# Kernel optimization log

Hardware: AMD Instinct MI355X
Metric: run time of the kernel (lower is better)

## Reference

```python
import jax, jax.numpy as jnp
import numpy as np
import math

SEQ_LEN = 2048
EMB = 1024
HEAD = 64
BATCH = 8

def setup_inputs() -> dict:
    key = jax.random.key(0)
    k1, k2, k3, k4 = jax.random.split(key, 4)
    x = jax.random.normal(k1, (BATCH, SEQ_LEN, EMB), dtype=jnp.float32)
    # torch Linear(no bias): out = x @ W.T with W [out,in]; store as [in,out]
    s = 1.0 / math.sqrt(EMB)
    Wk = jax.random.uniform(k2, (EMB, HEAD), dtype=jnp.float32, minval=-s, maxval=s)
    Wq = jax.random.uniform(k3, (EMB, HEAD), dtype=jnp.float32, minval=-s, maxval=s)
    Wv = jax.random.uniform(k4, (EMB, HEAD), dtype=jnp.float32, minval=-s, maxval=s)
    return {"x": x, "Wk": Wk, "Wq": Wq, "Wv": Wv}

def reference(x, Wk, Wq, Wv):
    B, S, E = x.shape
    H = Wk.shape[1]
    k = x @ Wk  # [B,S,H]
    q = x @ Wq
    v = x @ Wv
    scores = jnp.einsum('bsh,bth->bst', q, k) / math.sqrt(H)
    causal = jnp.tril(jnp.ones((S, S), dtype=bool))
    scores = jnp.where(causal[None], scores, -jnp.inf)
    attn = jax.nn.softmax(scores, axis=-1)
    # dropout is identity in eval mode
    return jnp.einsum('bst,bth->bsh', attn, v)
```

## Files before the change

### kernel.cpp

```cpp
#include <hip/hip_runtime.h>
#include <hip/hip_bf16.h>

typedef __attribute__((ext_vector_type(8))) short short8;
typedef __attribute__((ext_vector_type(4))) short short4v;
typedef __attribute__((ext_vector_type(4))) float floatx4;

#define SEQ   2048
#define EMB   1024
#define HEAD  64
#define BATCH 8

__device__ __forceinline__ short f2bf(float f) {
    union { float f; unsigned u; } a; a.f = f;
    unsigned u = a.u;
    u = (u + 0x7FFFu + ((u >> 16) & 1u)) >> 16;
    return (short)u;
}

__device__ __forceinline__ void gld16(const void* g, void* l) {
    __builtin_amdgcn_global_load_lds(
        (const __attribute__((address_space(1))) unsigned int*)g,
        (__attribute__((address_space(3))) unsigned int*)l,
        16, 0, 0);
}

__global__ void wtrans_kernel(const float* __restrict__ Wk,
                              const float* __restrict__ Wq,
                              const float* __restrict__ Wv,
                              short* __restrict__ Wf) {
    int gid  = blockIdx.x * 256 + threadIdx.x;
    int lane = gid & 63;
    int fid  = gid >> 6;
    int chunk = fid & 31;
    int mnt  = fid >> 5;
    int mat  = mnt >> 2, nt = mnt & 3;
    const float* src = (mat == 0) ? Wq : (mat == 1) ? Wk : Wv;
    int n = lane & 15, quad = lane >> 4;
    int h = nt * 16 + n;
    short8 o8;
    #pragma unroll
    for (int j = 0; j < 8; ++j)
        o8[j] = f2bf(src[(chunk * 32 + quad * 8 + j) * 64 + h]);
    *(short8*)(Wf + (long)gid * 8) = o8;
}

__global__ __launch_bounds__(256, 1) void qkv_kernel(const float* __restrict__ x,
                                                     const short* __restrict__ Wf,
                                                     short* __restrict__ q,
                                                     short* __restrict__ k,
                                                     short* __restrict__ vt) {
    __shared__ short LW[2][12][4][64][8];
    const int wv   = threadIdx.x >> 6;
    const int lane = threadIdx.x & 63;
    const int l15  = lane & 15;
    const int quad = lane >> 4;
    const int row0 = blockIdx.x * 64 + wv * 16;

    floatx4 acc[12];
    #pragma unroll
    for (int f = 0; f < 12; ++f) acc[f] = (floatx4){0.f, 0.f, 0.f, 0.f};

    const float* xrow = x + (long)(row0 + l15) * EMB + quad * 8;

    #pragma unroll
    for (int i = 0; i < 12; ++i) {
        const int s = wv * 12 + i, mnt = s >> 2, c = s & 3;
        gld16(Wf + (long)(mnt * 32 + c) * 512 + lane * 8, &LW[0][mnt][c][0][0]);
    }
    __syncthreads();

    #pragma unroll 1
    for (int g = 0; g < 8; ++g) {
        const int bb = g & 1;
        const float* xg = xrow + g * 128;
        floatx4 xv[8];
        #pragma unroll
        for (int c = 0; c < 4; ++c) {
            xv[2 * c]     = *(const floatx4*)(xg + c * 32);
            xv[2 * c + 1] = *(const floatx4*)(xg + c * 32 + 4);
        }
        if (g < 7) {
            #pragma unroll
            for (int i = 0; i < 12; ++i) {
                const int s = wv * 12 + i, mnt = s >> 2, c = s & 3;
                gld16(Wf + (long)(mnt * 32 + (g + 1) * 4 + c) * 512 + lane * 8,
                      &LW[bb ^ 1][mnt][c][0][0]);
            }
        }
        #pragma unroll
        for (int c = 0; c < 4; ++c) {
            short8 a;
            #pragma unroll
            for (int i = 0; i < 4; ++i) {
                a[i]     = f2bf(xv[2 * c][i]);
                a[4 + i] = f2bf(xv[2 * c + 1][i]);
            }
            #pragma unroll
            for (int f = 0; f < 12; ++f) {
                short8 bf = *(const short8*)&LW[bb][f][c][lane][0];
                acc[f] = __builtin_amdgcn_mfma_f32_16x16x32_bf16(a, bf, acc[f], 0, 0, 0);
            }
        }
        __syncthreads();
    }

    const int bidx = row0 >> 11;
    const int srow = (row0 & (SEQ - 1)) + quad * 4;
    #pragma unroll
    for (int nt = 0; nt < 4; ++nt) {
        const int col = nt * 16 + l15;
        #pragma unroll
        for (int r = 0; r < 4; ++r) {
            long grow = (long)(row0 + quad * 4 + r);
            q[grow * HEAD + col] = f2bf(acc[nt][r]);
            k[grow * HEAD + col] = f2bf(acc[4 + nt][r]);
        }
        short4v vv;
        #pragma unroll
        for (int r = 0; r < 4; ++r) vv[r] = f2bf(acc[8 + nt][r]);
        *(short4v*)(vt + ((long)bidx * HEAD + col) * SEQ + srow) = vv;
    }
}

__global__ __launch_bounds__(256, 2) void attn_kernel(const short* __restrict__ q,
                                                      const short* __restrict__ k,
                                                      const short* __restrict__ vt,
                                                      float* __restrict__ out) {
    __shared__ short KV[2][16][64][8];
    __shared__ short Plds[4][16][40];
    __shared__ float oT[2][2][16][64];
    __shared__ float lT[2][2][16];

    const int wv   = threadIdx.x >> 6;
    const int lane = threadIdx.x & 63;
    const int l15  = lane & 15;
    const int quad = lane >> 4;
    const int rg   = wv & 1;
    const int kh   = wv >> 1;
    const int b    = blockIdx.x & 7;
    const int p    = blockIdx.x >> 3;
    const int t2   = 63 - p;
    const int s1   = p * 32, s2 = t2 * 32;
    const int nch1 = (p >> 1) + 1;
    const int nch2 = (t2 >> 1) + 1;

    const short* kbase = k  + (long)b * SEQ * HEAD;
    const short* vbase = vt + (long)b * HEAD * SEQ;

    const short* q1p = q + ((long)b * SEQ + s1 + rg * 16 + l15) * HEAD + quad * 8;
    const short* q2p = q + ((long)b * SEQ + s2 + rg * 16 + l15) * HEAD + quad * 8;
    short8 q1f0 = *(const short8*)(q1p), q1f1 = *(const short8*)(q1p + 32);
    short8 q2f0 = *(const short8*)(q2p), q2f1 = *(const short8*)(q2p + 32);

    floatx4 o1[4], o2[4];
    #pragma unroll
    for (int nh = 0; nh < 4; ++nh) {
        o1[nh] = (floatx4){0.f, 0.f, 0.f, 0.f};
        o2[nh] = (floatx4){0.f, 0.f, 0.f, 0.f};
    }
    float l1[4] = {0.f, 0.f, 0.f, 0.f};
    float l2[4] = {0.f, 0.f, 0.f, 0.f};

    auto stage = [&](int ch, int bb) {
        const int j0 = ch * 64;
        #pragma unroll
        for (int i = 0; i < 2; ++i) {
            const int fid = wv + i * 4;
            const int ntg = fid >> 1, ks = fid & 1;
            gld16(kbase + (long)(j0 + ntg * 16 + l15) * HEAD + ks * 32 + quad * 8,
                  &KV[bb][fid][0][0]);
        }
        #pragma unroll
        for (int i = 0; i < 2; ++i) {
            const int fid = wv + i * 4;
            const int kh2 = fid >> 2, nth = fid & 3;
            gld16(vbase + (long)(nth * 16 + l15) * SEQ + j0 + kh2 * 32 + quad * 8,
                  &KV[bb][8 + fid][0][0]);
        }
    };

    stage(0, 0);
    __syncthreads();

    #pragma unroll 1
    for (int ch = 0; ch < nch2; ++ch) {
        const int bb = ch & 1;
        if (ch + 1 < nch2) stage(ch + 1, bb ^ 1);
        const int j0 = ch * 64;

        short8 kf[2][2], vf[4];
        #pragma unroll
        for (int nt = 0; nt < 2; ++nt)
            #pragma unroll
            for (int ks = 0; ks < 2; ++ks)
                kf[nt][ks] = *(const short8*)&KV[bb][(kh * 2 + nt) * 2 + ks][lane][0];
        #pragma unroll
        for (int nh = 0; nh < 4; ++nh)
            vf[nh] = *(const short8*)&KV[bb][8 + kh * 4 + nh][lane][0];

        {
            floatx4 sa[2];
            sa[0] = (floatx4){0.f, 0.f, 0.f, 0.f};
            sa[1] = (floatx4){0.f, 0.f, 0.f, 0.f};
            #pragma unroll
            for (int nt = 0; nt < 2; ++nt) {
                sa[nt] = __builtin_amdgcn_mfma_f32_16x16x32_bf16(q2f0, kf[nt][0], sa[nt], 0, 0, 0);
                sa[nt] = __builtin_amdgcn_mfma_f32_16x16x32_bf16(q2f1, kf[nt][1], sa[nt], 0, 0, 0);
            }
            #pragma unroll
            for (int r = 0; r < 4; ++r) {
                const int sq = s2 + rg * 16 + quad * 4 + r;
                #pragma unroll
                for (int nt = 0; nt < 2; ++nt) {
                    const int sk = j0 + kh * 32 + nt * 16 + l15;
                    float pv = (sk > sq) ? 0.f : __expf(sa[nt][r] * 0.125f - 16.f);
                    sa[nt][r] = pv;
                    l2[r] += pv;
                }
            }
            #pragma unroll
            for (int nt = 0; nt < 2; ++nt)
                #pragma unroll
                for (int r = 0; r < 4; ++r)
                    Plds[wv][quad * 4 + r][nt * 16 + l15] = f2bf(sa[nt][r]);
            short8 pf = *(const short8*)(&Plds[wv][l15][quad * 8]);
            #pragma unroll
            for (int nh = 0; nh < 4; ++nh)
                o2[nh] = __builtin_amdgcn_mfma_f32_16x16x32_bf16(pf, vf[nh], o2[nh], 0, 0, 0);
        }

        if (ch < nch1) {
            floatx4 sa[2];
            sa[0] = (floatx4){0.f, 0.f, 0.f, 0.f};
            sa[1] = (floatx4){0.f, 0.f, 0.f, 0.f};
            #pragma unroll
            for (int nt = 0; nt < 2; ++nt) {
                sa[nt] = __builtin_amdgcn_mfma_f32_16x16x32_bf16(q1f0, kf[nt][0], sa[nt], 0, 0, 0);
                sa[nt] = __builtin_amdgcn_mfma_f32_16x16x32_bf16(q1f1, kf[nt][1], sa[nt], 0, 0, 0);
            }
            #pragma unroll
            for (int r = 0; r < 4; ++r) {
                const int sq = s1 + rg * 16 + quad * 4 + r;
                #pragma unroll
                for (int nt = 0; nt < 2; ++nt) {
                    const int sk = j0 + kh * 32 + nt * 16 + l15;
                    float pv = (sk > sq) ? 0.f : __expf(sa[nt][r] * 0.125f - 16.f);
                    sa[nt][r] = pv;
                    l1[r] += pv;
                }
            }
            #pragma unroll
            for (int nt = 0; nt < 2; ++nt)
                #pragma unroll
                for (int r = 0; r < 4; ++r)
                    Plds[wv][quad * 4 + r][nt * 16 + l15] = f2bf(sa[nt][r]);
            short8 pf = *(const short8*)(&Plds[wv][l15][quad * 8]);
            #pragma unroll
            for (int nh = 0; nh < 4; ++nh)
                o1[nh] = __builtin_amdgcn_mfma_f32_16x16x32_bf16(pf, vf[nh], o1[nh], 0, 0, 0);
        }
        __syncthreads();
    }

    #pragma unroll
    for (int msk = 1; msk <= 8; msk <<= 1) {
        #pragma unroll
        for (int r = 0; r < 4; ++r) {
            l1[r] += __shfl_xor(l1[r], msk, 64);
            l2[r] += __shfl_xor(l2[r], msk, 64);
        }
    }

    if (kh == 1) {
        #pragma unroll
        for (int nh = 0; nh < 4; ++nh)
            #pragma unroll
            for (int r = 0; r < 4; ++r) {
                oT[0][rg][quad * 4 + r][nh * 16 + l15] = o1[nh][r];
                oT[1][rg][quad * 4 + r][nh * 16 + l15] = o2[nh][r];
            }
        if (l15 == 0) {
            #pragma unroll
            for (int r = 0; r < 4; ++r) {
                lT[0][rg][quad * 4 + r] = l1[r];
                lT[1][rg][quad * 4 + r] = l2[r];
            }
        }
    }
    __syncthreads();
    if (kh == 0) {
        #pragma unroll
        for (int r = 0; r < 4; ++r) {
            const int row = quad * 4 + r;
            const float inv1 = 1.f / (l1[r] + lT[0][rg][row]);
            const float inv2 = 1.f / (l2[r] + lT[1][rg][row]);
            #pragma unroll
            for (int nh = 0; nh < 4; ++nh) {
                const int col = nh * 16 + l15;
                out[((long)b * SEQ + s1 + rg * 16 + row) * HEAD + col] =
                    (o1[nh][r] + oT[0][rg][row][col]) * inv1;
                out[((long)b * SEQ + s2 + rg * 16 + row) * HEAD + col] =
                    (o2[nh][r] + oT[1][rg][row][col]) * inv2;
            }
        }
    }
}

extern "C" void kernel_launch(void* const* d_in, const int* in_sizes, int n_in,
                              void* d_out, int out_size, void* d_ws, size_t ws_size,
                              hipStream_t stream) {
    const float* x  = (const float*)d_in[0];
    const float* Wk = (const float*)d_in[1];
    const float* Wq = (const float*)d_in[2];
    const float* Wv = (const float*)d_in[3];
    float* out = (float*)d_out;

    short* Wf = (short*)d_ws;
    short* q  = Wf + 3 * HEAD * EMB;
    short* k  = q + (long)BATCH * SEQ * HEAD;
    short* vt = k + (long)BATCH * SEQ * HEAD;

    hipLaunchKernelGGL(wtrans_kernel, dim3(96), dim3(256), 0, stream, Wk, Wq, Wv, Wf);
    hipLaunchKernelGGL(qkv_kernel, dim3(BATCH * SEQ / 64), dim3(256), 0, stream, x, Wf, q, k, vt);
    hipLaunchKernelGGL(attn_kernel, dim3(BATCH * 32), dim3(256), 0, stream, q, k, vt, out);
}
```

Measured before the change: 158.4 us.

## Split QKV projection across waves per 16-row block and unpair attention tiles

The QKV projection kernel now gives each block 16 rows, with each wave computing 3 of the 12 output tiles. B fragments are read directly from global memory, replacing the LDS double-buffered staging, and the weight layout is reordered to suit. The attention kernel no longer pairs a short and a long query tile per block. It launches one block per 32-row tile, doubling the grid to 512 blocks, with the longest tiles scheduled first. bf16 conversion switches from round-to-nearest-even to a cheaper round-half-up. The aim is more parallelism and occupancy, at the cost of extra weight reads from L2 and more per-block overhead.

```diff
diff --git a/kernel.cpp b/kernel.cpp
--- a/kernel.cpp
+++ b/kernel.cpp
@@ -12,9 +12,19 @@
 
 __device__ __forceinline__ short f2bf(float f) {
     union { float f; unsigned u; } a; a.f = f;
-    unsigned u = a.u;
-    u = (u + 0x7FFFu + ((u >> 16) & 1u)) >> 16;
-    return (short)u;
+    return (short)((a.u + 0x8000u) >> 16);
+}
+
+__device__ __forceinline__ short8 pk8(floatx4 a, floatx4 b) {
+    short8 r;
+    #pragma unroll
+    for (int i = 0; i < 4; ++i) {
+        union { float f; unsigned u; } x1, x2;
+        x1.f = a[i]; x2.f = b[i];
+        r[i]     = (short)((x1.u + 0x8000u) >> 16);
+        r[4 + i] = (short)((x2.u + 0x8000u) >> 16);
+    }
+    return r;
 }
 
 __device__ __forceinline__ void gld16(const void* g, void* l) {
@@ -31,8 +41,8 @@
     int gid  = blockIdx.x * 256 + threadIdx.x;
     int lane = gid & 63;
     int fid  = gid >> 6;
-    int chunk = fid & 31;
-    int mnt  = fid >> 5;
+    int chunk = fid / 12;
+    int mnt  = fid - chunk * 12;
     int mat  = mnt >> 2, nt = mnt & 3;
     const float* src = (mat == 0) ? Wq : (mat == 1) ? Wk : Wv;
     int n = lane & 15, quad = lane >> 4;
@@ -44,81 +54,62 @@
     *(short8*)(Wf + (long)gid * 8) = o8;
 }
 
-__global__ __launch_bounds__(256, 1) void qkv_kernel(const float* __restrict__ x,
+__global__ __launch_bounds__(256, 4) void qkv_kernel(const float* __restrict__ x,
                                                      const short* __restrict__ Wf,
                                                      short* __restrict__ q,
                                                      short* __restrict__ k,
                                                      short* __restrict__ vt) {
-    __shared__ short LW[2][12][4][64][8];
     const int wv   = threadIdx.x >> 6;
     const int lane = threadIdx.x & 63;
     const int l15  = lane & 15;
     const int quad = lane >> 4;
-    const int row0 = blockIdx.x * 64 + wv * 16;
-
-    floatx4 acc[12];
-    #pragma unroll
-    for (int f = 0; f < 12; ++f) acc[f] = (floatx4){0.f, 0.f, 0.f, 0.f};
-
-    const float* xrow = x + (long)(row0 + l15) * EMB + quad * 8;
-
-    #pragma unroll
-    for (int i = 0; i < 12; ++i) {
-        const int s = wv * 12 + i, mnt = s >> 2, c = s & 3;
-        gld16(Wf + (long)(mnt * 32 + c) * 512 + lane * 8, &LW[0][mnt][c][0][0]);
-    }
-    __syncthreads();
-
-    #pragma unroll 1
-    for (int g = 0; g < 8; ++g) {
-        const int bb = g & 1;
-        const float* xg = xrow + g * 128;
-        floatx4 xv[8];
-        #pragma unroll
-        for (int c = 0; c < 4; ++c) {
-            xv[2 * c]     = *(const floatx4*)(xg + c * 32);
-            xv[2 * c + 1] = *(const floatx4*)(xg + c * 32 + 4);
-        }
-        if (g < 7) {
-            #pragma unroll
-            for (int i = 0; i < 12; ++i) {
-                const int s = wv * 12 + i, mnt = s >> 2, c = s & 3;
-                gld16(Wf + (long)(mnt * 32 + (g + 1) * 4 + c) * 512 + lane * 8,
-                      &LW[bb ^ 1][mnt][c][0][0]);
-            }
-        }
-        #pragma unroll
-        for (int c = 0; c < 4; ++c) {
-            short8 a;
-            #pragma unroll
-            for (int i = 0; i < 4; ++i) {
-                a[i]     = f2bf(xv[2 * c][i]);
-                a[4 + i] = f2bf(xv[2 * c + 1][i]);
-            }
-            #pragma unroll
-            for (int f = 0; f < 12; ++f) {
-                short8 bf = *(const short8*)&LW[bb][f][c][lane][0];
-                acc[f] = __builtin_amdgcn_mfma_f32_16x16x32_bf16(a, bf, acc[f], 0, 0, 0);
-            }
-        }
-        __syncthreads();
+    const int row0 = blockIdx.x * 16;
+    const int mnt0 = wv * 3;
+
+    floatx4 acc[3];
+    #pragma unroll
+    for (int i = 0; i < 3; ++i) acc[i] = (floatx4){0.f, 0.f, 0.f, 0.f};
+
+    const float* xrow  = x + (long)(row0 + l15) * EMB + quad * 8;
+    const short* wbase = Wf + ((long)mnt0 * 64 + lane) * 8;
+
+    #pragma unroll 2
+    for (int c = 0; c < 32; ++c) {
+        const float* xp = xrow + c * 32;
+        floatx4 xa = *(const floatx4*)(xp);
+        floatx4 xb = *(const floatx4*)(xp + 4);
+        const short* wp = wbase + (long)c * 12 * 512;
+        short8 b0 = *(const short8*)(wp);
+        short8 b1 = *(const short8*)(wp + 512);
+        short8 b2 = *(const short8*)(wp + 1024);
+        short8 a = pk8(xa, xb);
+        acc[0] = __builtin_amdgcn_mfma_f32_16x16x32_bf16(a, b0, acc[0], 0, 0, 0);
+        acc[1] = __builtin_amdgcn_mfma_f32_16x16x32_bf16(a, b1, acc[1], 0, 0, 0);
+        acc[2] = __builtin_amdgcn_mfma_f32_16x16x32_bf16(a, b2, acc[2], 0, 0, 0);
     }
 
     const int bidx = row0 >> 11;
-    const int srow = (row0 & (SEQ - 1)) + quad * 4;
-    #pragma unroll
-    for (int nt = 0; nt < 4; ++nt) {
-        const int col = nt * 16 + l15;
-        #pragma unroll
-        for (int r = 0; r < 4; ++r) {
-            long grow = (long)(row0 + quad * 4 + r);
-            q[grow * HEAD + col] = f2bf(acc[nt][r]);
-            k[grow * HEAD + col] = f2bf(acc[4 + nt][r]);
-        }
-        short4v vv;
-        #pragma unroll
-        for (int r = 0; r < 4; ++r) vv[r] = f2bf(acc[8 + nt][r]);
-        *(short4v*)(vt + ((long)bidx * HEAD + col) * SEQ + srow) = vv;
+    #pragma unroll
+    for (int i = 0; i < 3; ++i) {
+        const int mnt = mnt0 + i;
+        const int mat = mnt >> 2, ntl = mnt & 3;
+        const int col = ntl * 16 + l15;
+        const long rbase = row0 + quad * 4;
+        if (mat == 0) {
+            #pragma unroll
+            for (int r = 0; r < 4; ++r)
+                q[(rbase + r) * HEAD + col] = f2bf(acc[i][r]);
+        } else if (mat == 1) {
+            #pragma unroll
+            for (int r = 0; r < 4; ++r)
+                k[(rbase + r) * HEAD + col] = f2bf(acc[i][r]);
+        } else {
+            short4v vv;
+            #pragma unroll
+            for (int r = 0; r < 4; ++r) vv[r] = f2bf(acc[i][r]);
+            const int srow = (int)(rbase & (SEQ - 1));
+            *(short4v*)(vt + ((long)bidx * HEAD + col) * SEQ + srow) = vv;
+        }
     }
 }
 
@@ -128,8 +119,8 @@
                                                       float* __restrict__ out) {
     __shared__ short KV[2][16][64][8];
     __shared__ short Plds[4][16][40];
-    __shared__ float oT[2][2][16][64];
-    __shared__ float lT[2][2][16];
+    __shared__ float oT[2][16][64];
+    __shared__ float lT[2][16];
 
     const int wv   = threadIdx.x >> 6;
     const int lane = threadIdx.x & 63;
@@ -138,28 +129,20 @@
     const int rg   = wv & 1;
     const int kh   = wv >> 1;
     const int b    = blockIdx.x & 7;
-    const int p    = blockIdx.x >> 3;
-    const int t2   = 63 - p;
-    const int s1   = p * 32, s2 = t2 * 32;
-    const int nch1 = (p >> 1) + 1;
-    const int nch2 = (t2 >> 1) + 1;
+    const int t    = 63 - (blockIdx.x >> 3);
+    const int s0   = t * 32;
+    const int nch  = (t + 2) >> 1;
 
     const short* kbase = k  + (long)b * SEQ * HEAD;
     const short* vbase = vt + (long)b * HEAD * SEQ;
 
-    const short* q1p = q + ((long)b * SEQ + s1 + rg * 16 + l15) * HEAD + quad * 8;
-    const short* q2p = q + ((long)b * SEQ + s2 + rg * 16 + l15) * HEAD + quad * 8;
-    short8 q1f0 = *(const short8*)(q1p), q1f1 = *(const short8*)(q1p + 32);
-    short8 q2f0 = *(const short8*)(q2p), q2f1 = *(const short8*)(q2p + 32);
-
-    floatx4 o1[4], o2[4];
-    #pragma unroll
-    for (int nh = 0; nh < 4; ++nh) {
-        o1[nh] = (floatx4){0.f, 0.f, 0.f, 0.f};
-        o2[nh] = (floatx4){0.f, 0.f, 0.f, 0.f};
-    }
-    float l1[4] = {0.f, 0.f, 0.f, 0.f};
-    float l2[4] = {0.f, 0.f, 0.f, 0.f};
+    const short* qp = q + ((long)b * SEQ + s0 + rg * 16 + l15) * HEAD + quad * 8;
+    short8 qf0 = *(const short8*)(qp), qf1 = *(const short8*)(qp + 32);
+
+    floatx4 o[4];
+    #pragma unroll
+    for (int nh = 0; nh < 4; ++nh) o[nh] = (floatx4){0.f, 0.f, 0.f, 0.f};
+    float l_i[4] = {0.f, 0.f, 0.f, 0.f};
 
     auto stage = [&](int ch, int bb) {
         const int j0 = ch * 64;
@@ -183,9 +166,9 @@
     __syncthreads();
 
     #pragma unroll 1
-    for (int ch = 0; ch < nch2; ++ch) {
+    for (int ch = 0; ch < nch; ++ch) {
         const int bb = ch & 1;
-        if (ch + 1 < nch2) stage(ch + 1, bb ^ 1);
+        if (ch + 1 < nch) stage(ch + 1, bb ^ 1);
         const int j0 = ch * 64;
 
         short8 kf[2][2], vf[4];
@@ -198,93 +181,55 @@
         for (int nh = 0; nh < 4; ++nh)
             vf[nh] = *(const short8*)&KV[bb][8 + kh * 4 + nh][lane][0];
 
-        {
-            floatx4 sa[2];
-            sa[0] = (floatx4){0.f, 0.f, 0.f, 0.f};
-            sa[1] = (floatx4){0.f, 0.f, 0.f, 0.f};
+        floatx4 sa[2];
+        sa[0] = (floatx4){0.f, 0.f, 0.f, 0.f};
+        sa[1] = (floatx4){0.f, 0.f, 0.f, 0.f};
+        #pragma unroll
+        for (int nt = 0; nt < 2; ++nt) {
+            sa[nt] = __builtin_amdgcn_mfma_f32_16x16x32_bf16(qf0, kf[nt][0], sa[nt], 0, 0, 0);
+            sa[nt] = __builtin_amdgcn_mfma_f32_16x16x32_bf16(qf1, kf[nt][1], sa[nt], 0, 0, 0);
+        }
+        #pragma unroll
+        for (int r = 0; r < 4; ++r) {
+            const int sq = s0 + rg * 16 + quad * 4 + r;
             #pragma unroll
             for (int nt = 0; nt < 2; ++nt) {
-                sa[nt] = __builtin_amdgcn_mfma_f32_16x16x32_bf16(q2f0, kf[nt][0], sa[nt], 0, 0, 0);
-                sa[nt] = __builtin_amdgcn_mfma_f32_16x16x32_bf16(q2f1, kf[nt][1], sa[nt], 0, 0, 0);
+                const int sk = j0 + kh * 32 + nt * 16 + l15;
+                float pv = (sk > sq) ? 0.f : __expf(sa[nt][r] * 0.125f - 16.f);
+                sa[nt][r] = pv;
+                l_i[r] += pv;
             }
-            #pragma unroll
-            for (int r = 0; r < 4; ++r) {
-                const int sq = s2 + rg * 16 + quad * 4 + r;
-                #pragma unroll
-                for (int nt = 0; nt < 2; ++nt) {
-                    const int sk = j0 + kh * 32 + nt * 16 + l15;
-                    float pv = (sk > sq) ? 0.f : __expf(sa[nt][r] * 0.125f - 16.f);
-                    sa[nt][r] = pv;
-                    l2[r] += pv;
-                }
-            }
-            #pragma unroll
-            for (int nt = 0; nt < 2; ++nt)
-                #pragma unroll
-                for (int r = 0; r < 4; ++r)
-                    Plds[wv][quad * 4 + r][nt * 16 + l15] = f2bf(sa[nt][r]);
-            short8 pf = *(const short8*)(&Plds[wv][l15][quad * 8]);
-            #pragma unroll
-            for (int nh = 0; nh < 4; ++nh)
-                o2[nh] = __builtin_amdgcn_mfma_f32_16x16x32_bf16(pf, vf[nh], o2[nh], 0, 0, 0);
-        }
-
-        if (ch < nch1) {
-            floatx4 sa[2];
-            sa[0] = (floatx4){0.f, 0.f, 0.f, 0.f};
-            sa[1] = (floatx4){0.f, 0.f, 0.f, 0.f};
-            #pragma unroll
-            for (int nt = 0; nt < 2; ++nt) {
-                sa[nt] = __builtin_amdgcn_mfma_f32_16x16x32_bf16(q1f0, kf[nt][0], sa[nt], 0, 0, 0);
-                sa[nt] = __builtin_amdgcn_mfma_f32_16x16x32_bf16(q1f1, kf[nt][1], sa[nt], 0, 0, 0);
-            }
-            #pragma unroll
-            for (int r = 0; r < 4; ++r) {
-                const int sq = s1 + rg * 16 + quad * 4 + r;
-                #pragma unroll
-                for (int nt = 0; nt < 2; ++nt) {
-                    const int sk = j0 + kh * 32 + nt * 16 + l15;
-                    float pv = (sk > sq) ? 0.f : __expf(sa[nt][r] * 0.125f - 16.f);
-                    sa[nt][r] = pv;
-                    l1[r] += pv;
-                }
-            }
-            #pragma unroll
-            for (int nt = 0; nt < 2; ++nt)
-                #pragma unroll
-                for (int r = 0; r < 4; ++r)
-                    Plds[wv][quad * 4 + r][nt * 16 + l15] = f2bf(sa[nt][r]);
-            short8 pf = *(const short8*)(&Plds[wv][l15][quad * 8]);
-            #pragma unroll
-            for (int nh = 0; nh < 4; ++nh)
-                o1[nh] = __builtin_amdgcn_mfma_f32_16x16x32_bf16(pf, vf[nh], o1[nh], 0, 0, 0);
-        }
+        }
+        #pragma unroll
+        for (int nt = 0; nt < 2; ++nt)
+            #pragma unroll
+            for (int r = 0; r < 4; ++r)
+                Plds[wv][quad * 4 + r][nt * 16 + l15] = f2bf(sa[nt][r]);
+        short8 pf = *(const short8*)(&Plds[wv][l15][quad * 8]);
+        #pragma unroll
+        for (int nh = 0; nh < 4; ++nh)
+            o[nh] = __builtin_amdgcn_mfma_f32_16x16x32_bf16(pf, vf[nh], o[nh], 0, 0, 0);
+
         __syncthreads();
     }
 
     #pragma unroll
     for (int msk = 1; msk <= 8; msk <<= 1) {
         #pragma unroll
-        for (int r = 0; r < 4; ++r) {
-            l1[r] += __shfl_xor(l1[r], msk, 64);
-            l2[r] += __shfl_xor(l2[r], msk, 64);
-        }
+        for (int r = 0; r < 4; ++r)
+            l_i[r] += __shfl_xor(l_i[r], msk, 64);
     }
 
     if (kh == 1) {
         #pragma unroll
         for (int nh = 0; nh < 4; ++nh)
             #pragma unroll
-            for (int r = 0; r < 4; ++r) {
-                oT[0][rg][quad * 4 + r][nh * 16 + l15] = o1[nh][r];
-                oT[1][rg][quad * 4 + r][nh * 16 + l15] = o2[nh][r];
-            }
+            for (int r = 0; r < 4; ++r)
+                oT[rg][quad * 4 + r][nh * 16 + l15] = o[nh][r];
         if (l15 == 0) {
             #pragma unroll
-            for (int r = 0; r < 4; ++r) {
-                lT[0][rg][quad * 4 + r] = l1[r];
-                lT[1][rg][quad * 4 + r] = l2[r];
-            }
+            for (int r = 0; r < 4; ++r)
+                lT[rg][quad * 4 + r] = l_i[r];
         }
     }
     __syncthreads();
@@ -292,15 +237,12 @@
         #pragma unroll
         for (int r = 0; r < 4; ++r) {
             const int row = quad * 4 + r;
-            const float inv1 = 1.f / (l1[r] + lT[0][rg][row]);
-            const float inv2 = 1.f / (l2[r] + lT[1][rg][row]);
+            const float inv = 1.f / (l_i[r] + lT[rg][row]);
             #pragma unroll
             for (int nh = 0; nh < 4; ++nh) {
                 const int col = nh * 16 + l15;
-                out[((long)b * SEQ + s1 + rg * 16 + row) * HEAD + col] =
-                    (o1[nh][r] + oT[0][rg][row][col]) * inv1;
-                out[((long)b * SEQ + s2 + rg * 16 + row) * HEAD + col] =
-                    (o2[nh][r] + oT[1][rg][row][col]) * inv2;
+                out[((long)b * SEQ + s0 + rg * 16 + row) * HEAD + col] =
+                    (o[nh][r] + oT[rg][row][col]) * inv;
             }
         }
     }
@@ -321,6 +263,6 @@
     short* vt = k + (long)BATCH * SEQ * HEAD;
 
     hipLaunchKernelGGL(wtrans_kernel, dim3(96), dim3(256), 0, stream, Wk, Wq, Wv, Wf);
-    hipLaunchKernelGGL(qkv_kernel, dim3(BATCH * SEQ / 64), dim3(256), 0, stream, x, Wf, q, k, vt);
-    hipLaunchKernelGGL(attn_kernel, dim3(BATCH * 32), dim3(256), 0, stream, q, k, vt, out);
-}
+    hipLaunchKernelGGL(qkv_kernel, dim3(BATCH * SEQ / 16), dim3(256), 0, stream, x, Wf, q, k, vt);
+    hipLaunchKernelGGL(attn_kernel, dim3(BATCH * 64), dim3(256), 0, stream, q, k, vt, out);
+}
```

Result: slower. 169.3 us (+6.9%).
